# Kernel optimization log

Measured on AMD Instinct MI355X. Metric: run time of the kernel, lower is better.

Reference implementation:

```python
import jax, jax.numpy as jnp
import numpy as np

HEADS = 16

def setup_inputs() -> dict:
    key = jax.random.key(0)
    ks = jax.random.split(key, 4)
    emb = 1024
    x = jax.random.normal(ks[0], (2, 2048, emb), dtype=jnp.float32)
    Wqkv = jax.random.normal(ks[1], (emb, 3 * emb), dtype=jnp.float32) * 0.02
    bqkv = jnp.zeros((3 * emb,), dtype=jnp.float32)
    Wproj = jax.random.normal(ks[2], (emb, emb), dtype=jnp.float32) * 0.02
    bproj = jnp.zeros((emb,), dtype=jnp.float32)
    return {"x": x, "Wqkv": Wqkv, "bqkv": bqkv, "Wproj": Wproj, "bproj": bproj}


def reference(x, Wqkv, bqkv, Wproj, bproj):
    b, n, e = x.shape
    h = HEADS
    d = e // h
    # qkv projection; last dim factors as (h, d, 3): q/k/v interleaved innermost,
    # matching einops rearrange 'b n (h d q) -> q b h n d'
    t = (x @ Wqkv + bqkv).reshape(b, n, h, d, 3)
    q, k, v = t[..., 0], t[..., 1], t[..., 2]  # each [b, n, h, d]
    scale = np.float32(1.0 / np.sqrt(e))  # note: sqrt(emb), not sqrt(head_dim)
    att = jax.nn.softmax(jnp.einsum('bnhd,bmhd->bhnm', q, k) * scale, axis=-1)
    out = jnp.einsum('bhnm,bmhd->bnhd', att, v).reshape(b, n, e)
    return out @ Wproj + bproj
```

## Files before the change

kernel.cpp:

```cpp
#include <hip/hip_runtime.h>

typedef __bf16 bf16;
typedef __attribute__((ext_vector_type(8))) __bf16 bf16x8;
typedef __attribute__((ext_vector_type(4))) float f32x4;
typedef __attribute__((ext_vector_type(16))) float f32x16;
typedef unsigned int u32;
typedef __attribute__((ext_vector_type(2))) unsigned int u32x2;
typedef __attribute__((ext_vector_type(4))) unsigned int u32x4;

#define SEQ 2048
#define EMB 1024
#define NH  16
#define DH  64

__global__ __launch_bounds__(256) void prep(const float* __restrict__ x, bf16* __restrict__ xb,
                                            const float* __restrict__ Wqkv, bf16* __restrict__ WqkvT,
                                            const float* __restrict__ Wproj, bf16* __restrict__ WprojT) {
    __shared__ float t[32][33];
    int b = blockIdx.x;
    if (b < 2048) {
        int i = b * 256 + threadIdx.x;
        float4 a = ((const float4*)x)[2 * i];
        float4 c = ((const float4*)x)[2 * i + 1];
        bf16x8 o;
        o[0] = (bf16)a.x; o[1] = (bf16)a.y; o[2] = (bf16)a.z; o[3] = (bf16)a.w;
        o[4] = (bf16)c.x; o[5] = (bf16)c.y; o[6] = (bf16)c.z; o[7] = (bf16)c.w;
        ((bf16x8*)xb)[i] = o;
        return;
    }
    int tx = threadIdx.x & 31, ty = threadIdx.x >> 5;
    if (b < 5120) {
        int flat = b - 2048;
        int c0 = (flat % 96) * 32, r0 = (flat / 96) * 32;
#pragma unroll
        for (int s = 0; s < 4; s++) {
            int row = ty + s * 8;
            t[row][tx] = Wqkv[(size_t)(r0 + row) * 3072 + c0 + tx];
        }
        __syncthreads();
#pragma unroll
        for (int s = 0; s < 4; s++) {
            int row = ty + s * 8;
            int corig = c0 + row;
            int hh = corig / 192;
            int rem = corig - hh * 192;
            int dd = rem / 3;
            int which = rem - dd * 3;
            int colp = which * 1024 + hh * 64 + dd;
            WqkvT[(size_t)colp * EMB + r0 + tx] = (bf16)t[tx][row];
        }
    } else {
        int flat = b - 5120;
        int c0 = (flat % 32) * 32, r0 = (flat / 32) * 32;
#pragma unroll
        for (int s = 0; s < 4; s++) {
            int row = ty + s * 8;
            t[row][tx] = Wproj[(size_t)(r0 + row) * EMB + c0 + tx];
        }
        __syncthreads();
#pragma unroll
        for (int s = 0; s < 4; s++) {
            int row = ty + s * 8;
            WprojT[(size_t)(c0 + row) * EMB + r0 + tx] = (bf16)t[tx][row];
        }
    }
}


#define BM 128
#define BN 128
#define BK 32

__device__ __forceinline__ void gload16(const bf16* g, bf16* l) {
    __builtin_amdgcn_global_load_lds((__attribute__((address_space(1))) void*)(void*)g,
                                     (__attribute__((address_space(3))) void*)l, 16, 0, 0);
}

__device__ __forceinline__ void stage_tile(const bf16* src, int ld, int row0, int k0,
                                           bf16* lds, int wave, int lane) {
#pragma unroll
    for (int c = 0; c < 2; c++) {
        int chunk = wave + 4 * c;
        int row = chunk * 16 + (lane >> 2);
        int slot = (lane & 3) ^ ((lane >> 2) & 3);
        const bf16* g = src + (size_t)(row0 + row) * ld + k0 + slot * 8;
        gload16(g, lds + chunk * 512);
    }
}

__device__ __forceinline__ bf16x8 frag(const bf16* lds, int row, int s) {
    int slot = s ^ (row & 3);
    return *(const bf16x8*)&lds[row * BK + slot * 8];
}

__device__ __forceinline__ void gemm_mainloop(const bf16* A, const bf16* Bt, int Kdim,
                                              int m0, int n0, bf16* As, bf16* Bs,
                                              int wave, int lane, int wr, int wc,
                                              f32x4 acc[4][4]) {
    stage_tile(A, Kdim, m0, 0, As, wave, lane);
    stage_tile(Bt, Kdim, n0, 0, Bs, wave, lane);
    asm volatile("s_waitcnt vmcnt(0)" ::: "memory");
    __builtin_amdgcn_s_barrier();

    int cur = 0;
    const int iters = Kdim / BK;
    for (int it = 0; it < iters; ++it) {
        if (it + 1 < iters) {
            stage_tile(A, Kdim, m0, (it + 1) * BK, As + (cur ^ 1) * BM * BK, wave, lane);
            stage_tile(Bt, Kdim, n0, (it + 1) * BK, Bs + (cur ^ 1) * BN * BK, wave, lane);
        }
        const bf16* as = As + cur * BM * BK;
        const bf16* bs = Bs + cur * BN * BK;
        int s = lane >> 4;
        bf16x8 a[4], b[4];
#pragma unroll
        for (int i = 0; i < 4; i++)
            a[i] = frag(as, wr * 64 + i * 16 + (lane & 15), s);
#pragma unroll
        for (int j = 0; j < 4; j++)
            b[j] = frag(bs, wc * 64 + j * 16 + (lane & 15), s);
#pragma unroll
        for (int i = 0; i < 4; i++)
#pragma unroll
            for (int j = 0; j < 4; j++)
                acc[i][j] = __builtin_amdgcn_mfma_f32_16x16x32_bf16(a[i], b[j], acc[i][j], 0, 0, 0);
        asm volatile("s_waitcnt vmcnt(0)" ::: "memory");
        __builtin_amdgcn_s_barrier();
        cur ^= 1;
    }
}

__global__ __launch_bounds__(256) void gemm_qkv(const bf16* __restrict__ A,
                                                const bf16* __restrict__ Bt,
                                                const float* __restrict__ bias,
                                                bf16* __restrict__ Qb, bf16* __restrict__ Kb,
                                                bf16* __restrict__ Vt) {
    __shared__ alignas(16) bf16 smem[4 * BM * BK];
    bf16* As = smem;
    bf16* Bs = smem + 2 * BM * BK;
    int wave = threadIdx.x >> 6, lane = threadIdx.x & 63;
    int wr = wave >> 1, wc = wave & 1;

    int flat = blockIdx.y * 24 + blockIdx.x;
    int swz = (flat & 7) * 96 + (flat >> 3);
    int n0 = (swz % 24) * BN;
    int m0 = (swz / 24) * BM;

    f32x4 acc[4][4] = {};
    gemm_mainloop(A, Bt, EMB, m0, n0, As, Bs, wave, lane, wr, wc, acc);

    int which = n0 >> 10;
    bool isV = (which == 2);
    char* tile = (char*)smem;

#pragma unroll
    for (int i = 0; i < 4; i++) {
#pragma unroll
        for (int j = 0; j < 4; j++) {
            int c = wc * 64 + j * 16 + (lane & 15);
            int hh = ((n0 + c) >> 6) & 15;
            int dd = c & 63;
            float bv = bias[hh * 192 + dd * 3 + which];
#pragma unroll
            for (int r = 0; r < 4; r++) {
                int rowL = wr * 64 + i * 16 + 4 * (lane >> 4) + r;
                float v = acc[i][j][r] + bv;
                if (which == 0) v *= 0.03125f;
                int byte;
                if (!isV) byte = rowL * 256 + ((c * 2) ^ ((rowL & 7) << 4));
                else      byte = c * 256 + ((((rowL >> 3) ^ (c & 15)) << 4) + (rowL & 7) * 2);
                *(bf16*)(tile + byte) = (bf16)v;
            }
        }
    }
    __builtin_amdgcn_s_barrier();

    int tid = threadIdx.x;
    if (which == 0) {
#pragma unroll
        for (int k = 0; k < 8; k++) {
            int f = k * 256 + tid;
            int rowL = f >> 4, ch = f & 15;
            bf16x8 val = *(const bf16x8*)(tile + rowL * 256 + ((ch ^ (rowL & 7)) << 4));
            int grow = m0 + rowL;
            int bb = grow >> 11, npos = grow & 2047;
            int cbase = ch * 8;
            int hh = ((n0 + cbase) >> 6) & 15;
            int d0 = cbase & 63;
            *(bf16x8*)(Qb + (((size_t)bb * NH + hh) * SEQ + npos) * DH + d0) = val;
        }
    } else if (which == 1) {
#pragma unroll
        for (int k = 0; k < 8; k++) {
            int f = k * 256 + tid;
            int rowL = f >> 4, ch = f & 15;
            bf16x8 val = *(const bf16x8*)(tile + rowL * 256 + ((ch ^ (rowL & 7)) << 4));
            int grow = m0 + rowL;
            int bb = grow >> 11, npos = grow & 2047;
            int cbase = ch * 8;
            int hh = ((n0 + cbase) >> 6) & 15;
            int d0 = cbase & 63;
            size_t base = ((size_t)bb * NH + hh) * (SEQ * DH) + (size_t)(npos >> 6) * 4096;
            int chunk = ((npos >> 5) & 1) * 8 + (d0 >> 4) * 2 + ((d0 >> 3) & 1);
            *(bf16x8*)(Kb + base + chunk * 256 + (npos & 31) * 8) = val;
        }
    } else {
#pragma unroll
        for (int k = 0; k < 8; k++) {
            int f = k * 256 + tid;
            int cL = f >> 4, g = f & 15;
            bf16x8 val = *(const bf16x8*)(tile + cL * 256 + ((g ^ (cL & 15)) << 4));
            int grow = m0 + g * 8;
            int bb = grow >> 11, nn = grow & 2047;
            int hh = ((n0 + cL) >> 6) & 15;
            int d = cL & 63;
            int tIdx = nn >> 6;
            int mb = nn & 63;
            int mc = mb >> 4, half = (mb >> 3) & 1;
            char* base = (char*)Vt +
                         (((size_t)bb * NH + hh) * (SEQ * DH) + (size_t)tIdx * 4096) * 2;
            u32x4 vv = __builtin_bit_cast(u32x4, val);
            u32x2 lo = {vv.x, vv.y};
            u32x2 hi = {vv.z, vv.w};
            int off = ((d >> 5) * 4 + mc) * 1024 + (d & 31) * 16 + half * 8;
            *(u32x2*)(base + off) = lo;
            *(u32x2*)(base + off + 512) = hi;
        }
    }
}

__global__ __launch_bounds__(256) void gemm_proj(const bf16* __restrict__ A,
                                                 const bf16* __restrict__ Bt,
                                                 const float* __restrict__ bias,
                                                 float* __restrict__ C) {
    __shared__ alignas(16) bf16 smem[4 * BM * BK];
    bf16* As = smem;
    bf16* Bs = smem + 2 * BM * BK;
    int wave = threadIdx.x >> 6, lane = threadIdx.x & 63;
    int wr = wave >> 1, wc = wave & 1;
    int m0 = blockIdx.y * BM, n0 = blockIdx.x * BN;
    f32x4 acc[4][4] = {};
    gemm_mainloop(A, Bt, EMB, m0, n0, As, Bs, wave, lane, wr, wc, acc);

    int m_base = m0 + wr * 64;
    int n_base = n0 + wc * 64;
#pragma unroll
    for (int i = 0; i < 4; i++) {
#pragma unroll
        for (int j = 0; j < 4; j++) {
            int col = n_base + j * 16 + (lane & 15);
            float bv = bias[col];
#pragma unroll
            for (int r = 0; r < 4; r++) {
                int row = m_base + i * 16 + 4 * (lane >> 4) + r;
                C[(size_t)row * EMB + col] = acc[i][j][r] + bv;
            }
        }
    }
}


__device__ __forceinline__ void stage16k(const bf16* src, bf16* lds, int wave, int lane) {
#pragma unroll
    for (int i = 0; i < 4; i++) {
        int c = wave * 4 + i;
        gload16(src + c * 512 + lane * 8, lds + c * 512);
    }
}

__device__ __forceinline__ u32 pack_bf16(float lo, float hi) {
    unsigned short a = __builtin_bit_cast(unsigned short, (bf16)lo);
    unsigned short b = __builtin_bit_cast(unsigned short, (bf16)hi);
    return (u32)a | ((u32)b << 16);
}

__global__ __launch_bounds__(256, 2) void attn(const bf16* __restrict__ Q,
                                               const bf16* __restrict__ K,
                                               const bf16* __restrict__ Vt,
                                               bf16* __restrict__ O) {
    int flat = blockIdx.x;
    int swz = (flat & 7) * 64 + (flat >> 3);
    int bh = swz >> 4;
    int qb = swz & 15;

    int wave = threadIdx.x >> 6, lane = threadIdx.x & 63;
    int l31 = lane & 31, h = lane >> 5;
    int qw0 = qb * 128 + wave * 32;
    const bf16* Qg = Q + (size_t)bh * SEQ * DH;
    const bf16* Kg = K + (size_t)bh * SEQ * DH;
    const bf16* Vg = Vt + (size_t)bh * SEQ * DH;

    __shared__ alignas(16) bf16 Ks[2][8192];

    bf16x8 qf[4];
#pragma unroll
    for (int ks = 0; ks < 4; ks++)
        qf[ks] = *(const bf16x8*)(Qg + (size_t)(qw0 + l31) * DH + ks * 16 + h * 8);

    f32x16 Oc[2] = {};
    float lsum = 0.f;

    stage16k(Kg, &Ks[0][0], wave, lane);
    asm volatile("s_waitcnt vmcnt(0)" ::: "memory");
    __builtin_amdgcn_s_barrier();

    int cur = 0;
    const int NIT = SEQ / 128;
    for (int it = 0; it < NIT; ++it) {
        if (it + 1 < NIT) {
            stage16k(Kg + (size_t)(it + 1) * 8192, &Ks[cur ^ 1][0], wave, lane);
        }
        const char* kc = (const char*)&Ks[cur][0];
        const bf16* vgi = Vg + (size_t)it * 8192;

        u32 w[4][8];
        float part[4];
#pragma unroll
        for (int T = 0; T < 4; T++) {
            bf16x8 kf[4];
#pragma unroll
            for (int ks = 0; ks < 4; ks++)
                kf[ks] = *(const bf16x8*)(kc + (((T * 4 + ks) * 2 + h) << 9) + l31 * 16);
            f32x16 st = {};
#pragma unroll
            for (int ks = 0; ks < 4; ks++)
                st = __builtin_amdgcn_mfma_f32_32x32x16_bf16(kf[ks], qf[ks], st, 0, 0, 0);
            float acc = 0.f;
#pragma unroll
            for (int p = 0; p < 8; p++) {
                float p0 = __expf(st[2 * p]);
                float p1 = __expf(st[2 * p + 1]);
                acc += p0 + p1;
                w[T][p] = pack_bf16(p0, p1);
            }
            part[T] = acc;
        }
        lsum += (part[0] + part[1]) + (part[2] + part[3]);

#pragma unroll
        for (int mg = 0; mg < 2; mg++)
#pragma unroll
            for (int dt = 0; dt < 2; dt++)
#pragma unroll
                for (int mc = 0; mc < 4; mc++) {
                    bf16x8 vf = *(const bf16x8*)(vgi + mg * 4096 +
                                                 ((dt * 4 + mc) * 2 + h) * 256 + l31 * 8);
                    int Tw = mg * 2 + (mc >> 1);
                    u32x4 pw = {w[Tw][4 * (mc & 1) + 0], w[Tw][4 * (mc & 1) + 1],
                                w[Tw][4 * (mc & 1) + 2], w[Tw][4 * (mc & 1) + 3]};
                    bf16x8 pa = __builtin_bit_cast(bf16x8, pw);
                    Oc[dt] = __builtin_amdgcn_mfma_f32_32x32x16_bf16(pa, vf, Oc[dt], 0, 0, 0);
                }

        asm volatile("s_waitcnt vmcnt(0)" ::: "memory");
        __builtin_amdgcn_s_barrier();
        cur ^= 1;
    }

    float ls = lsum + __shfl_xor(lsum, 32);
    float rinv = 1.0f / ls;
    int bb = bh >> 4, hh = bh & 15;
#pragma unroll
    for (int reg = 0; reg < 16; reg++) {
        int qlocal = (reg & 3) + 8 * (reg >> 2) + 4 * h;
        float sc = __shfl(rinv, qlocal);
        int row = qw0 + qlocal;
#pragma unroll
        for (int dt = 0; dt < 2; dt++) {
            O[((size_t)bb * SEQ + row) * EMB + hh * DH + dt * 32 + l31] =
                (bf16)(Oc[dt][reg] * sc);
        }
    }
}


extern "C" void kernel_launch(void* const* d_in, const int* in_sizes, int n_in,
                              void* d_out, int out_size, void* d_ws, size_t ws_size,
                              hipStream_t stream) {
    const float* x     = (const float*)d_in[0];
    const float* Wqkv  = (const float*)d_in[1];
    const float* bqkv  = (const float*)d_in[2];
    const float* Wproj = (const float*)d_in[3];
    const float* bproj = (const float*)d_in[4];
    float* out = (float*)d_out;
    char* ws = (char*)d_ws;

    bf16* xb     = (bf16*)(ws + 0);
    bf16* attO   = xb;
    bf16* WqkvT  = (bf16*)(ws + 8388608);
    bf16* WprojT = (bf16*)(ws + 14680064);
    bf16* Qb     = (bf16*)(ws + 16777216);
    bf16* Kb     = (bf16*)(ws + 25165824);
    bf16* Vt     = (bf16*)(ws + 33554432);

    prep<<<6144, 256, 0, stream>>>(x, xb, Wqkv, WqkvT, Wproj, WprojT);
    gemm_qkv<<<dim3(24, 32), 256, 0, stream>>>(xb, WqkvT, bqkv, Qb, Kb, Vt);
    attn<<<512, 256, 0, stream>>>(Qb, Kb, Vt, attO);
    gemm_proj<<<dim3(8, 32), 256, 0, stream>>>(attO, WprojT, bproj, out);
}
```

Measured before the change: 133.2 us.

## Split attention KV sequence across two wave groups per block with LDS reduction

```diff
diff --git a/kernel.cpp b/kernel.cpp
--- a/kernel.cpp
+++ b/kernel.cpp
@@ -260,10 +260,10 @@
 }
 
 
-__device__ __forceinline__ void stage16k(const bf16* src, bf16* lds, int wave, int lane) {
+__device__ __forceinline__ void stage16k(const bf16* src, bf16* lds, int wg, int lane) {
 #pragma unroll
     for (int i = 0; i < 4; i++) {
-        int c = wave * 4 + i;
+        int c = wg * 4 + i;
         gload16(src + c * 512 + lane * 8, lds + c * 512);
     }
 }
@@ -274,7 +274,7 @@
     return (u32)a | ((u32)b << 16);
 }
 
-__global__ __launch_bounds__(256, 2) void attn(const bf16* __restrict__ Q,
+__global__ __launch_bounds__(512, 4) void attn(const bf16* __restrict__ Q,
                                                const bf16* __restrict__ K,
                                                const bf16* __restrict__ Vt,
                                                bf16* __restrict__ O) {
@@ -284,13 +284,14 @@
     int qb = swz & 15;
 
     int wave = threadIdx.x >> 6, lane = threadIdx.x & 63;
+    int wg = wave & 3, half = wave >> 2;
     int l31 = lane & 31, h = lane >> 5;
-    int qw0 = qb * 128 + wave * 32;
+    int qw0 = qb * 128 + wg * 32;
     const bf16* Qg = Q + (size_t)bh * SEQ * DH;
-    const bf16* Kg = K + (size_t)bh * SEQ * DH;
-    const bf16* Vg = Vt + (size_t)bh * SEQ * DH;
-
-    __shared__ alignas(16) bf16 Ks[2][8192];
+    const bf16* Kg = K + (size_t)bh * SEQ * DH + half * 65536;
+    const bf16* Vg = Vt + (size_t)bh * SEQ * DH + half * 65536;
+
+    __shared__ alignas(16) bf16 Ks[2][2][8192];
 
     bf16x8 qf[4];
 #pragma unroll
@@ -300,17 +301,17 @@
     f32x16 Oc[2] = {};
     float lsum = 0.f;
 
-    stage16k(Kg, &Ks[0][0], wave, lane);
+    stage16k(Kg, &Ks[half][0][0], wg, lane);
     asm volatile("s_waitcnt vmcnt(0)" ::: "memory");
     __builtin_amdgcn_s_barrier();
 
     int cur = 0;
-    const int NIT = SEQ / 128;
+    const int NIT = 8;
     for (int it = 0; it < NIT; ++it) {
         if (it + 1 < NIT) {
-            stage16k(Kg + (size_t)(it + 1) * 8192, &Ks[cur ^ 1][0], wave, lane);
-        }
-        const char* kc = (const char*)&Ks[cur][0];
+            stage16k(Kg + (size_t)(it + 1) * 8192, &Ks[half][cur ^ 1][0], wg, lane);
+        }
+        const char* kc = (const char*)&Ks[half][cur][0];
         const bf16* vgi = Vg + (size_t)it * 8192;
 
         u32 w[4][8];
@@ -322,9 +323,11 @@
             for (int ks = 0; ks < 4; ks++)
                 kf[ks] = *(const bf16x8*)(kc + (((T * 4 + ks) * 2 + h) << 9) + l31 * 16);
             f32x16 st = {};
+            __builtin_amdgcn_s_setprio(1);
 #pragma unroll
             for (int ks = 0; ks < 4; ks++)
                 st = __builtin_amdgcn_mfma_f32_32x32x16_bf16(kf[ks], qf[ks], st, 0, 0, 0);
+            __builtin_amdgcn_s_setprio(0);
             float acc = 0.f;
 #pragma unroll
             for (int p = 0; p < 8; p++) {
@@ -337,6 +340,7 @@
         }
         lsum += (part[0] + part[1]) + (part[2] + part[3]);
 
+        __builtin_amdgcn_s_setprio(1);
 #pragma unroll
         for (int mg = 0; mg < 2; mg++)
 #pragma unroll
@@ -351,24 +355,43 @@
                     bf16x8 pa = __builtin_bit_cast(bf16x8, pw);
                     Oc[dt] = __builtin_amdgcn_mfma_f32_32x32x16_bf16(pa, vf, Oc[dt], 0, 0, 0);
                 }
+        __builtin_amdgcn_s_setprio(0);
 
         asm volatile("s_waitcnt vmcnt(0)" ::: "memory");
         __builtin_amdgcn_s_barrier();
         cur ^= 1;
     }
 
-    float ls = lsum + __shfl_xor(lsum, 32);
-    float rinv = 1.0f / ls;
-    int bb = bh >> 4, hh = bh & 15;
-#pragma unroll
-    for (int reg = 0; reg < 16; reg++) {
-        int qlocal = (reg & 3) + 8 * (reg >> 2) + 4 * h;
-        float sc = __shfl(rinv, qlocal);
-        int row = qw0 + qlocal;
-#pragma unroll
-        for (int dt = 0; dt < 2; dt++) {
-            O[((size_t)bb * SEQ + row) * EMB + hh * DH + dt * 32 + l31] =
-                (bf16)(Oc[dt][reg] * sc);
+    float* cb = (float*)&Ks[0][0][0];
+    int cbase = (wg * 64 + lane) * 33;
+    if (half == 1) {
+#pragma unroll
+        for (int k = 0; k < 16; k++) cb[cbase + k] = Oc[0][k];
+#pragma unroll
+        for (int k = 0; k < 16; k++) cb[cbase + 16 + k] = Oc[1][k];
+        cb[cbase + 32] = lsum;
+    }
+    __syncthreads();
+    if (half == 0) {
+#pragma unroll
+        for (int k = 0; k < 16; k++) Oc[0][k] += cb[cbase + k];
+#pragma unroll
+        for (int k = 0; k < 16; k++) Oc[1][k] += cb[cbase + 16 + k];
+        lsum += cb[cbase + 32];
+
+        float ls = lsum + __shfl_xor(lsum, 32);
+        float rinv = 1.0f / ls;
+        int bb = bh >> 4, hh = bh & 15;
+#pragma unroll
+        for (int reg = 0; reg < 16; reg++) {
+            int qlocal = (reg & 3) + 8 * (reg >> 2) + 4 * h;
+            float sc = __shfl(rinv, qlocal);
+            int row = qw0 + qlocal;
+#pragma unroll
+            for (int dt = 0; dt < 2; dt++) {
+                O[((size_t)bb * SEQ + row) * EMB + hh * DH + dt * 32 + l31] =
+                    (bf16)(Oc[dt][reg] * sc);
+            }
         }
     }
 }
@@ -395,6 +418,6 @@
 
     prep<<<6144, 256, 0, stream>>>(x, xb, Wqkv, WqkvT, Wproj, WprojT);
     gemm_qkv<<<dim3(24, 32), 256, 0, stream>>>(xb, WqkvT, bqkv, Qb, Kb, Vt);
-    attn<<<512, 256, 0, stream>>>(Qb, Kb, Vt, attO);
+    attn<<<512, 512, 0, stream>>>(Qb, Kb, Vt, attO);
     gemm_proj<<<dim3(8, 32), 256, 0, stream>>>(attO, WprojT, bproj, out);
 }
```

New measurement: 265.4 us. 1.99x slower.

## Triple-buffer GEMM tiles, stage V through LDS in attention, add MFMA priority hints

Applied to the files above, without the earlier changes.

```diff
diff --git a/kernel.cpp b/kernel.cpp
--- a/kernel.cpp
+++ b/kernel.cpp
@@ -97,20 +97,24 @@
                                               int m0, int n0, bf16* As, bf16* Bs,
                                               int wave, int lane, int wr, int wc,
                                               f32x4 acc[4][4]) {
+    const int iters = Kdim / BK;
     stage_tile(A, Kdim, m0, 0, As, wave, lane);
     stage_tile(Bt, Kdim, n0, 0, Bs, wave, lane);
-    asm volatile("s_waitcnt vmcnt(0)" ::: "memory");
+    stage_tile(A, Kdim, m0, BK, As + BM * BK, wave, lane);
+    stage_tile(Bt, Kdim, n0, BK, Bs + BM * BK, wave, lane);
+    asm volatile("s_waitcnt vmcnt(4)" ::: "memory");
     __builtin_amdgcn_s_barrier();
 
-    int cur = 0;
-    const int iters = Kdim / BK;
     for (int it = 0; it < iters; ++it) {
-        if (it + 1 < iters) {
-            stage_tile(A, Kdim, m0, (it + 1) * BK, As + (cur ^ 1) * BM * BK, wave, lane);
-            stage_tile(Bt, Kdim, n0, (it + 1) * BK, Bs + (cur ^ 1) * BN * BK, wave, lane);
+        int cur = it % 3;
+        bool more = (it + 2 < iters);
+        if (more) {
+            int nxt = (it + 2) % 3;
+            stage_tile(A, Kdim, m0, (it + 2) * BK, As + nxt * BM * BK, wave, lane);
+            stage_tile(Bt, Kdim, n0, (it + 2) * BK, Bs + nxt * BM * BK, wave, lane);
         }
         const bf16* as = As + cur * BM * BK;
-        const bf16* bs = Bs + cur * BN * BK;
+        const bf16* bs = Bs + cur * BM * BK;
         int s = lane >> 4;
         bf16x8 a[4], b[4];
 #pragma unroll
@@ -124,9 +128,11 @@
 #pragma unroll
             for (int j = 0; j < 4; j++)
                 acc[i][j] = __builtin_amdgcn_mfma_f32_16x16x32_bf16(a[i], b[j], acc[i][j], 0, 0, 0);
-        asm volatile("s_waitcnt vmcnt(0)" ::: "memory");
+        if (more)
+            asm volatile("s_waitcnt vmcnt(4)" ::: "memory");
+        else
+            asm volatile("s_waitcnt vmcnt(0)" ::: "memory");
         __builtin_amdgcn_s_barrier();
-        cur ^= 1;
     }
 }
 
@@ -135,9 +141,9 @@
                                                 const float* __restrict__ bias,
                                                 bf16* __restrict__ Qb, bf16* __restrict__ Kb,
                                                 bf16* __restrict__ Vt) {
-    __shared__ alignas(16) bf16 smem[4 * BM * BK];
+    __shared__ alignas(16) bf16 smem[6 * BM * BK];
     bf16* As = smem;
-    bf16* Bs = smem + 2 * BM * BK;
+    bf16* Bs = smem + 3 * BM * BK;
     int wave = threadIdx.x >> 6, lane = threadIdx.x & 63;
     int wr = wave >> 1, wc = wave & 1;
 
@@ -152,6 +158,7 @@
     int which = n0 >> 10;
     bool isV = (which == 2);
     char* tile = (char*)smem;
+    __builtin_amdgcn_s_barrier();
 
 #pragma unroll
     for (int i = 0; i < 4; i++) {
@@ -233,9 +240,9 @@
                                                  const bf16* __restrict__ Bt,
                                                  const float* __restrict__ bias,
                                                  float* __restrict__ C) {
-    __shared__ alignas(16) bf16 smem[4 * BM * BK];
+    __shared__ alignas(16) bf16 smem[6 * BM * BK];
     bf16* As = smem;
-    bf16* Bs = smem + 2 * BM * BK;
+    bf16* Bs = smem + 3 * BM * BK;
     int wave = threadIdx.x >> 6, lane = threadIdx.x & 63;
     int wr = wave >> 1, wc = wave & 1;
     int m0 = blockIdx.y * BM, n0 = blockIdx.x * BN;
@@ -291,6 +298,7 @@
     const bf16* Vg = Vt + (size_t)bh * SEQ * DH;
 
     __shared__ alignas(16) bf16 Ks[2][8192];
+    __shared__ alignas(16) bf16 Vs[2][8192];
 
     bf16x8 qf[4];
 #pragma unroll
@@ -301,6 +309,7 @@
     float lsum = 0.f;
 
     stage16k(Kg, &Ks[0][0], wave, lane);
+    stage16k(Vg, &Vs[0][0], wave, lane);
     asm volatile("s_waitcnt vmcnt(0)" ::: "memory");
     __builtin_amdgcn_s_barrier();
 
@@ -309,9 +318,10 @@
     for (int it = 0; it < NIT; ++it) {
         if (it + 1 < NIT) {
             stage16k(Kg + (size_t)(it + 1) * 8192, &Ks[cur ^ 1][0], wave, lane);
+            stage16k(Vg + (size_t)(it + 1) * 8192, &Vs[cur ^ 1][0], wave, lane);
         }
         const char* kc = (const char*)&Ks[cur][0];
-        const bf16* vgi = Vg + (size_t)it * 8192;
+        const char* vc = (const char*)&Vs[cur][0];
 
         u32 w[4][8];
         float part[4];
@@ -322,9 +332,11 @@
             for (int ks = 0; ks < 4; ks++)
                 kf[ks] = *(const bf16x8*)(kc + (((T * 4 + ks) * 2 + h) << 9) + l31 * 16);
             f32x16 st = {};
+            __builtin_amdgcn_s_setprio(1);
 #pragma unroll
             for (int ks = 0; ks < 4; ks++)
                 st = __builtin_amdgcn_mfma_f32_32x32x16_bf16(kf[ks], qf[ks], st, 0, 0, 0);
+            __builtin_amdgcn_s_setprio(0);
             float acc = 0.f;
 #pragma unroll
             for (int p = 0; p < 8; p++) {
@@ -337,20 +349,22 @@
         }
         lsum += (part[0] + part[1]) + (part[2] + part[3]);
 
+        __builtin_amdgcn_s_setprio(1);
 #pragma unroll
         for (int mg = 0; mg < 2; mg++)
 #pragma unroll
             for (int dt = 0; dt < 2; dt++)
 #pragma unroll
                 for (int mc = 0; mc < 4; mc++) {
-                    bf16x8 vf = *(const bf16x8*)(vgi + mg * 4096 +
-                                                 ((dt * 4 + mc) * 2 + h) * 256 + l31 * 8);
+                    bf16x8 vf = *(const bf16x8*)(vc + mg * 8192 +
+                                                 (((dt * 4 + mc) * 2 + h) << 9) + l31 * 16);
                     int Tw = mg * 2 + (mc >> 1);
                     u32x4 pw = {w[Tw][4 * (mc & 1) + 0], w[Tw][4 * (mc & 1) + 1],
                                 w[Tw][4 * (mc & 1) + 2], w[Tw][4 * (mc & 1) + 3]};
                     bf16x8 pa = __builtin_bit_cast(bf16x8, pw);
                     Oc[dt] = __builtin_amdgcn_mfma_f32_32x32x16_bf16(pa, vf, Oc[dt], 0, 0, 0);
                 }
+        __builtin_amdgcn_s_setprio(0);
 
         asm volatile("s_waitcnt vmcnt(0)" ::: "memory");
         __builtin_amdgcn_s_barrier();
```

Result: faster. 118.9 us (-10.7%).
